# Optimization experiments

Measured on AMD Instinct MI355X. Metric: run time of the kernel, lower is better.

## Reference

```python
import jax, jax.numpy as jnp
import numpy as np

B, T, C = 16, 2048, 1024
HEAD = 64

def setup_inputs() -> dict:
    key = jax.random.key(0)
    kx, kq, kk, kv = jax.random.split(key, 4)
    x = jax.random.normal(kx, (B, T, C), dtype=jnp.float32)
    s = 1.0 / np.sqrt(C)
    Wq = jax.random.normal(kq, (C, HEAD), dtype=jnp.float32) * s
    Wk = jax.random.normal(kk, (C, HEAD), dtype=jnp.float32) * s
    Wv = jax.random.normal(kv, (C, HEAD), dtype=jnp.float32) * s
    return {"x": x, "Wq": Wq, "Wk": Wk, "Wv": Wv}

def reference(x, Wq, Wk, Wv):
    Bb, Tt, Cc = x.shape
    q = jnp.einsum('btc,ch->bth', x, Wq)  # [B,T,H]
    k = jnp.einsum('btc,ch->bth', x, Wk)
    v = jnp.einsum('btc,ch->bth', x, Wv)
    # NOTE: source scales by C**-0.5 (n_embd), not head_size**-0.5
    scores = jnp.einsum('bth,bsh->bts', q, k) * (Cc ** -0.5)  # [B,T,T]
    causal = jnp.tril(jnp.ones((Tt, Tt), dtype=bool))
    scores = jnp.where(causal, scores, -jnp.inf)
    attn = jax.nn.softmax(scores, axis=-1)  # dropout p=0 -> identity
    out = jnp.einsum('bts,bsh->bth', attn, v)  # [B,T,H]
    return out
```

## Files before the change

kernel.cpp:

```cpp
#include <hip/hip_runtime.h>

typedef __bf16 bf16;
typedef __bf16 bf16x2 __attribute__((ext_vector_type(2)));
typedef __bf16 bf16x4 __attribute__((ext_vector_type(4)));
typedef __bf16 bf16x8 __attribute__((ext_vector_type(8)));
typedef float f32x4 __attribute__((ext_vector_type(4)));

#define TT_ 2048
#define CC_ 1024
#define HH_ 64

#define SCALE2 0.045084221f

static __device__ __forceinline__ unsigned pack_bf16(float a, float b) {
    union { bf16x2 h; unsigned u; } z;
    z.h = bf16x2{(bf16)a, (bf16)b};
    return z.u;
}
static __device__ __forceinline__ void plswap32(unsigned &a, unsigned &b) {
    asm("v_permlane32_swap_b32 %0, %1" : "+v"(a), "+v"(b));
}
static __device__ __forceinline__ void plswap16(unsigned &a, unsigned &b) {
    asm("v_permlane16_swap_b32 %0, %1" : "+v"(a), "+v"(b));
}

__global__ __launch_bounds__(256) void prep_w(const float* __restrict__ Wq,
                                              const float* __restrict__ Wk,
                                              const float* __restrict__ Wv,
                                              bf16* __restrict__ Wt) {
    __shared__ bf16 Ls[64 * 65];
    const int m  = blockIdx.x >> 4;
    const int k0 = (blockIdx.x & 15) * 64;
    const float* W = (m == 0) ? Wq : (m == 1) ? Wk : Wv;
    const int tid = threadIdx.x;
    #pragma unroll
    for (int j = 0; j < 4; ++j) {
        int idx = tid + 256 * j;
        int r   = idx >> 4;
        int c4  = (idx & 15) * 4;
        float4 w = *(const float4*)&W[(size_t)(k0 + r) * HH_ + c4];
        Ls[r * 65 + c4 + 0] = (bf16)w.x;
        Ls[r * 65 + c4 + 1] = (bf16)w.y;
        Ls[r * 65 + c4 + 2] = (bf16)w.z;
        Ls[r * 65 + c4 + 3] = (bf16)w.w;
    }
    __syncthreads();
    #pragma unroll
    for (int j = 0; j < 4; ++j) {
        int idx = tid + 256 * j;
        int n   = idx >> 4;
        int kc  = (idx & 15) * 4;
        bf16x4 v;
        #pragma unroll
        for (int i = 0; i < 4; ++i) v[i] = Ls[(kc + i) * 65 + n];
        *(bf16x4*)&Wt[m * 65536 + n * 1024 + k0 + kc] = v;
    }
}

#define QKV_STEP(KBI, BU, BP, XLD, XWR)                                        \
    {                                                                          \
        const int k0 = (KBI) * 64;                                             \
        __syncthreads();                                                       \
        if ((KBI) < 14) {                                                      \
            _Pragma("unroll")                                                  \
            for (int rr = 0; rr < 4; ++rr)                                     \
                XLD[rr] = *(const float4*)&x[(size_t)(m0 + srow + rr * 16) * CC_ + k0 + 128 + scol]; \
        }                                                                      \
        if ((KBI) < 15) {                                                      \
            _Pragma("unroll")                                                  \
            for (int step = 0; step < 2; ++step)                               \
                _Pragma("unroll")                                              \
                for (int ct = 0; ct < 3; ++ct)                                 \
                    BP[step][ct] = *(const bf16x8*)&Wt[(size_t)(wave * 48 + ct * 16 + lane) * 1024 + k0 + 64 + step * 32 + quad * 8]; \
        }                                                                      \
        bf16x8 afr[2][4];                                                      \
        _Pragma("unroll")                                                      \
        for (int step = 0; step < 2; ++step)                                   \
            _Pragma("unroll")                                                  \
            for (int rt = 0; rt < 4; ++rt)                                     \
                afr[step][rt] = *(const bf16x8*)&Xs[(KBI) & 1][(rt * 16 + lane) * 72 + step * 32 + quad * 8]; \
        _Pragma("unroll")                                                      \
        for (int step = 0; step < 2; ++step)                                   \
            _Pragma("unroll")                                                  \
            for (int ct = 0; ct < 3; ++ct)                                     \
                _Pragma("unroll")                                              \
                for (int rt = 0; rt < 4; ++rt)                                 \
                    acc[rt][ct] = __builtin_amdgcn_mfma_f32_16x16x32_bf16(afr[step][rt], BU[step][ct], acc[rt][ct], 0, 0, 0); \
        if ((KBI) < 15) {                                                      \
            _Pragma("unroll")                                                  \
            for (int rr = 0; rr < 4; ++rr) {                                   \
                bf16x4 bv = {(bf16)XWR[rr].x, (bf16)XWR[rr].y, (bf16)XWR[rr].z, (bf16)XWR[rr].w}; \
                *(bf16x4*)&Xs[((KBI) + 1) & 1][(srow + rr * 16) * 72 + scol] = bv; \
            }                                                                  \
        }                                                                      \
    }

__global__ __launch_bounds__(256, 2) void qkv_kernel(const float* __restrict__ x,
                                                     const bf16* __restrict__ Wt,
                                                     bf16* __restrict__ qb,
                                                     bf16* __restrict__ kb,
                                                     bf16* __restrict__ vt) {
    __shared__ __align__(16) bf16 Xs[2][64 * 72];
    const int tid  = threadIdx.x;
    const int wave = tid >> 6;
    const int lane = tid & 15;
    const int quad = (tid & 63) >> 4;
    const int m0   = blockIdx.x * 64;

    f32x4 acc[4][3];
    #pragma unroll
    for (int i = 0; i < 4; ++i)
        #pragma unroll
        for (int j = 0; j < 3; ++j) acc[i][j] = f32x4{0.f, 0.f, 0.f, 0.f};

    const int srow = tid >> 4;
    const int scol = (tid & 15) * 4;

    {
        float4 x0[4];
        #pragma unroll
        for (int rr = 0; rr < 4; ++rr)
            x0[rr] = *(const float4*)&x[(size_t)(m0 + srow + rr * 16) * CC_ + scol];
        #pragma unroll
        for (int rr = 0; rr < 4; ++rr) {
            bf16x4 bv = {(bf16)x0[rr].x, (bf16)x0[rr].y, (bf16)x0[rr].z, (bf16)x0[rr].w};
            *(bf16x4*)&Xs[0][(srow + rr * 16) * 72 + scol] = bv;
        }
    }
    float4 xS0[4], xS1[4];
    #pragma unroll
    for (int rr = 0; rr < 4; ++rr)
        xS1[rr] = *(const float4*)&x[(size_t)(m0 + srow + rr * 16) * CC_ + 64 + scol];
    bf16x8 bfrA[2][3], bfrB[2][3];
    #pragma unroll
    for (int step = 0; step < 2; ++step)
        #pragma unroll
        for (int ct = 0; ct < 3; ++ct)
            bfrA[step][ct] = *(const bf16x8*)&Wt[(size_t)(wave * 48 + ct * 16 + lane) * 1024 + step * 32 + quad * 8];

    for (int kb2 = 0; kb2 < 16; kb2 += 2) {
        QKV_STEP(kb2,     bfrA, bfrB, xS0, xS1)
        QKV_STEP(kb2 + 1, bfrB, bfrA, xS1, xS0)
    }

    const int bb = m0 >> 11;
    const int t0 = m0 & 2047;
    __syncthreads();
    #pragma unroll
    for (int ct = 0; ct < 3; ++ct) {
        int c0 = wave * 48 + ct * 16;
        if (c0 < 64) {
            int h = c0 + lane;
            #pragma unroll
            for (int rt = 0; rt < 4; ++rt)
                #pragma unroll
                for (int r = 0; r < 4; ++r)
                    qb[(size_t)(m0 + rt * 16 + quad * 4 + r) * HH_ + h] = (bf16)(acc[rt][ct][r] * SCALE2);
        } else if (c0 < 128) {
            int h = (c0 - 64) + lane;
            #pragma unroll
            for (int rt = 0; rt < 4; ++rt)
                #pragma unroll
                for (int r = 0; r < 4; ++r)
                    kb[(size_t)(m0 + rt * 16 + quad * 4 + r) * HH_ + h] = (bf16)acc[rt][ct][r];
        } else {
            int h = (c0 - 128) + lane;
            #pragma unroll
            for (int rt = 0; rt < 4; ++rt)
                #pragma unroll
                for (int r = 0; r < 4; ++r)
                    Xs[0][(rt * 16 + quad * 4 + r) * 72 + h] = (bf16)acc[rt][ct][r];
        }
    }
    __syncthreads();
    {
        int h  = tid >> 2;
        int tc = (tid & 3) * 16;
        bf16x8 v0, v1;
        #pragma unroll
        for (int i = 0; i < 8; ++i) v0[i] = Xs[0][(tc + i) * 72 + h];
        #pragma unroll
        for (int i = 0; i < 8; ++i) v1[i] = Xs[0][(tc + 8 + i) * 72 + h];
        bf16* dst = &vt[(size_t)bb * HH_ * TT_ + (size_t)h * TT_ + t0 + tc];
        *(bf16x8*)dst = v0;
        *(bf16x8*)(dst + 8) = v1;
    }
}

__global__ __launch_bounds__(256, 2) void attn_kernel(const bf16* __restrict__ qb,
                                                      const bf16* __restrict__ kb,
                                                      const bf16* __restrict__ vt,
                                                      float* __restrict__ out) {
    __shared__ __align__(16) bf16 Ks[2][128 * 72];
    __shared__ __align__(16) bf16 Vs[2][64 * 136];

    const int tid  = threadIdx.x;
    const int wave = tid >> 6;
    const int lane = tid & 15;
    const int quad = (tid & 63) >> 4;

    const int j  = blockIdx.x;
    const int bb = j & 15;
    const int p  = j >> 4;
    const int qi = (p < 16) ? p : 47 - p;
    const int nch = (qi >> 1) + 1;

    const int qrow  = qi * 64 + wave * 16;
    const int qg    = qrow + lane;
    const int qmaxw = qrow + 15;

    const int krow = tid >> 3, kc8 = (tid & 7) * 8;
    const int vh   = tid >> 4, vc8 = (tid & 15) * 8;
    const bf16* kp = kb + (size_t)(bb * TT_ + krow) * HH_ + kc8;
    const bf16* vp = vt + (size_t)bb * HH_ * TT_ + (size_t)vh * TT_ + vc8;

    bf16x8 kr[4], vvr[4];
    #pragma unroll
    for (int j2 = 0; j2 < 4; ++j2) kr[j2]  = *(const bf16x8*)&kp[(size_t)j2 * 32 * HH_];
    #pragma unroll
    for (int j2 = 0; j2 < 4; ++j2) vvr[j2] = *(const bf16x8*)&vp[j2 * 16 * TT_];
    #pragma unroll
    for (int j2 = 0; j2 < 4; ++j2) *(bf16x8*)&Ks[0][(krow + 32 * j2) * 72 + kc8] = kr[j2];
    #pragma unroll
    for (int j2 = 0; j2 < 4; ++j2) *(bf16x8*)&Vs[0][(vh + 16 * j2) * 136 + vc8]  = vvr[j2];
    __syncthreads();

    bf16x8 aq[2];
    #pragma unroll
    for (int step = 0; step < 2; ++step)
        aq[step] = *(const bf16x8*)&qb[(size_t)(bb * TT_ + qg) * HH_ + step * 32 + quad * 8];

    bf16x8 vones;
    #pragma unroll
    for (int i = 0; i < 8; ++i) vones[i] = (bf16)1.0f;

    f32x4 o_acc[4];
    #pragma unroll
    for (int ht = 0; ht < 4; ++ht) o_acc[ht] = f32x4{0.f, 0.f, 0.f, 0.f};
    f32x4 lacc = f32x4{0.f, 0.f, 0.f, 0.f};

    for (int c = 0; c < nch; ++c) {
        const int s0  = c * 128;
        const int cur = c & 1;
        if (c + 1 < nch) {
            #pragma unroll
            for (int j2 = 0; j2 < 4; ++j2)
                kr[j2] = *(const bf16x8*)&kp[(size_t)((c + 1) * 128 + j2 * 32) * HH_];
            #pragma unroll
            for (int j2 = 0; j2 < 4; ++j2)
                vvr[j2] = *(const bf16x8*)&vp[(c + 1) * 128 + j2 * 16 * TT_];
        }

        const bool msk = (c == nch - 1);
        #pragma unroll
        for (int w = 0; w < 4; ++w) {
            if (msk && (s0 + w * 32 > qmaxw)) continue;
            const bool haveB = !msk || (s0 + w * 32 + 16 <= qmaxw);

            f32x4 sA = {0.f, 0.f, 0.f, 0.f};
            f32x4 sB = {0.f, 0.f, 0.f, 0.f};
            __builtin_amdgcn_s_setprio(1);
            {
                bf16x8 ak0 = *(const bf16x8*)&Ks[cur][(w * 32 + lane) * 72 + quad * 8];
                bf16x8 ak1 = *(const bf16x8*)&Ks[cur][(w * 32 + lane) * 72 + 32 + quad * 8];
                sA = __builtin_amdgcn_mfma_f32_16x16x32_bf16(ak0, aq[0], sA, 0, 0, 0);
                sA = __builtin_amdgcn_mfma_f32_16x16x32_bf16(ak1, aq[1], sA, 0, 0, 0);
            }
            if (haveB) {
                bf16x8 bk0 = *(const bf16x8*)&Ks[cur][(w * 32 + 16 + lane) * 72 + quad * 8];
                bf16x8 bk1 = *(const bf16x8*)&Ks[cur][(w * 32 + 16 + lane) * 72 + 32 + quad * 8];
                sB = __builtin_amdgcn_mfma_f32_16x16x32_bf16(bk0, aq[0], sB, 0, 0, 0);
                sB = __builtin_amdgcn_mfma_f32_16x16x32_bf16(bk1, aq[1], sB, 0, 0, 0);
            }
            __builtin_amdgcn_s_setprio(0);

            const int kA0 = s0 + w * 32 + quad * 4;
            float eA[4], eB[4];
            #pragma unroll
            for (int r = 0; r < 4; ++r) {
                float e = __builtin_amdgcn_exp2f(sA[r]);
                if (msk && (kA0 + r > qg)) e = 0.f;
                eA[r] = e;
            }
            if (haveB) {
                #pragma unroll
                for (int r = 0; r < 4; ++r) {
                    float e = __builtin_amdgcn_exp2f(sB[r]);
                    if (msk && (kA0 + 16 + r > qg)) e = 0.f;
                    eB[r] = e;
                }
            } else {
                #pragma unroll
                for (int r = 0; r < 4; ++r) eB[r] = 0.f;
            }

            unsigned d0 = pack_bf16(eA[0], eA[1]);
            unsigned d1 = pack_bf16(eA[2], eA[3]);
            unsigned d2 = pack_bf16(eB[0], eB[1]);
            unsigned d3 = pack_bf16(eB[2], eB[3]);
            plswap32(d0, d2);
            plswap16(d0, d2);
            plswap32(d1, d3);
            plswap16(d1, d3);
            union { unsigned u[4]; bf16x8 v; } apu;
            apu.u[0] = d0; apu.u[1] = d1; apu.u[2] = d2; apu.u[3] = d3;

            __builtin_amdgcn_s_setprio(1);
            #pragma unroll
            for (int ht = 0; ht < 4; ++ht) {
                bf16x8 bv = *(const bf16x8*)&Vs[cur][(ht * 16 + lane) * 136 + w * 32 + quad * 8];
                o_acc[ht] = __builtin_amdgcn_mfma_f32_16x16x32_bf16(apu.v, bv, o_acc[ht], 0, 0, 0);
            }
            lacc = __builtin_amdgcn_mfma_f32_16x16x32_bf16(apu.v, vones, lacc, 0, 0, 0);
            __builtin_amdgcn_s_setprio(0);
        }

        if (c + 1 < nch) {
            #pragma unroll
            for (int j2 = 0; j2 < 4; ++j2) *(bf16x8*)&Ks[cur ^ 1][(krow + 32 * j2) * 72 + kc8] = kr[j2];
            #pragma unroll
            for (int j2 = 0; j2 < 4; ++j2) *(bf16x8*)&Vs[cur ^ 1][(vh + 16 * j2) * 136 + vc8]  = vvr[j2];
            __syncthreads();
        }
    }

    float inv[4];
    #pragma unroll
    for (int r = 0; r < 4; ++r) inv[r] = __builtin_amdgcn_rcpf(lacc[r]);
    #pragma unroll
    for (int ht = 0; ht < 4; ++ht)
        #pragma unroll
        for (int r = 0; r < 4; ++r)
            out[(size_t)(bb * TT_ + qrow + quad * 4 + r) * HH_ + ht * 16 + lane] = o_acc[ht][r] * inv[r];
}

extern "C" void kernel_launch(void* const* d_in, const int* in_sizes, int n_in,
                              void* d_out, int out_size, void* d_ws, size_t ws_size,
                              hipStream_t stream) {
    const float* x  = (const float*)d_in[0];
    const float* Wq = (const float*)d_in[1];
    const float* Wk = (const float*)d_in[2];
    const float* Wv = (const float*)d_in[3];
    float* out = (float*)d_out;

    char* ws = (char*)d_ws;
    bf16*  qb = (bf16*)(ws);
    bf16*  kb = (bf16*)(ws + 4194304);
    bf16*  vt = (bf16*)(ws + 8388608);
    bf16*  Wt = (bf16*)(ws + 12582912);

    prep_w<<<48, 256, 0, stream>>>(Wq, Wk, Wv, Wt);
    qkv_kernel<<<512, 256, 0, stream>>>(x, Wt, qb, kb, vt);
    attn_kernel<<<512, 256, 0, stream>>>(qb, kb, vt, out);
}
```

Baseline: 238.5 us.

## Split key chunks across two wave groups in attention and reduce via LDS

Doubles the attention block to 512 threads: four query waves are paired with two key groups, and each group handles alternating 32-key sub-tiles of every 128-key chunk. Partial output and row-sum accumulators are then combined through shared memory before normalisation. The aim is more waves per block to hide latency and to halve the serial per-wave work on the long causal rows. The cost is an extra LDS reduction with two barriers, and the launch-bounds change to (512,4) constrains register allocation more tightly.

```diff
diff --git a/kernel.cpp b/kernel.cpp
--- a/kernel.cpp
+++ b/kernel.cpp
@@ -187,7 +187,7 @@
     }
 }
 
-__global__ __launch_bounds__(256, 2) void attn_kernel(const bf16* __restrict__ qb,
+__global__ __launch_bounds__(512, 4) void attn_kernel(const bf16* __restrict__ qb,
                                                       const bf16* __restrict__ kb,
                                                       const bf16* __restrict__ vt,
                                                       float* __restrict__ out) {
@@ -196,6 +196,8 @@
 
     const int tid  = threadIdx.x;
     const int wave = tid >> 6;
+    const int qw   = wave & 3;
+    const int kg   = wave >> 2;
     const int lane = tid & 15;
     const int quad = (tid & 63) >> 4;
 
@@ -205,7 +207,7 @@
     const int qi = (p < 16) ? p : 47 - p;
     const int nch = (qi >> 1) + 1;
 
-    const int qrow  = qi * 64 + wave * 16;
+    const int qrow  = qi * 64 + qw * 16;
     const int qg    = qrow + lane;
     const int qmaxw = qrow + 15;
 
@@ -214,15 +216,15 @@
     const bf16* kp = kb + (size_t)(bb * TT_ + krow) * HH_ + kc8;
     const bf16* vp = vt + (size_t)bb * HH_ * TT_ + (size_t)vh * TT_ + vc8;
 
-    bf16x8 kr[4], vvr[4];
-    #pragma unroll
-    for (int j2 = 0; j2 < 4; ++j2) kr[j2]  = *(const bf16x8*)&kp[(size_t)j2 * 32 * HH_];
-    #pragma unroll
-    for (int j2 = 0; j2 < 4; ++j2) vvr[j2] = *(const bf16x8*)&vp[j2 * 16 * TT_];
-    #pragma unroll
-    for (int j2 = 0; j2 < 4; ++j2) *(bf16x8*)&Ks[0][(krow + 32 * j2) * 72 + kc8] = kr[j2];
-    #pragma unroll
-    for (int j2 = 0; j2 < 4; ++j2) *(bf16x8*)&Vs[0][(vh + 16 * j2) * 136 + vc8]  = vvr[j2];
+    bf16x8 kr[2], vvr[2];
+    #pragma unroll
+    for (int j2 = 0; j2 < 2; ++j2) kr[j2]  = *(const bf16x8*)&kp[(size_t)j2 * 64 * HH_];
+    #pragma unroll
+    for (int j2 = 0; j2 < 2; ++j2) vvr[j2] = *(const bf16x8*)&vp[j2 * 32 * TT_];
+    #pragma unroll
+    for (int j2 = 0; j2 < 2; ++j2) *(bf16x8*)&Ks[0][(krow + 64 * j2) * 72 + kc8] = kr[j2];
+    #pragma unroll
+    for (int j2 = 0; j2 < 2; ++j2) *(bf16x8*)&Vs[0][(vh + 32 * j2) * 136 + vc8]  = vvr[j2];
     __syncthreads();
 
     bf16x8 aq[2];
@@ -244,16 +246,17 @@
         const int cur = c & 1;
         if (c + 1 < nch) {
             #pragma unroll
-            for (int j2 = 0; j2 < 4; ++j2)
-                kr[j2] = *(const bf16x8*)&kp[(size_t)((c + 1) * 128 + j2 * 32) * HH_];
-            #pragma unroll
-            for (int j2 = 0; j2 < 4; ++j2)
-                vvr[j2] = *(const bf16x8*)&vp[(c + 1) * 128 + j2 * 16 * TT_];
+            for (int j2 = 0; j2 < 2; ++j2)
+                kr[j2] = *(const bf16x8*)&kp[(size_t)((c + 1) * 128 + j2 * 64) * HH_];
+            #pragma unroll
+            for (int j2 = 0; j2 < 2; ++j2)
+                vvr[j2] = *(const bf16x8*)&vp[(c + 1) * 128 + j2 * 32 * TT_];
         }
 
         const bool msk = (c == nch - 1);
         #pragma unroll
-        for (int w = 0; w < 4; ++w) {
+        for (int wi = 0; wi < 2; ++wi) {
+            const int w = kg + wi * 2;
             if (msk && (s0 + w * 32 > qmaxw)) continue;
             const bool haveB = !msk || (s0 + w * 32 + 16 <= qmaxw);
 
@@ -317,21 +320,44 @@
 
         if (c + 1 < nch) {
             #pragma unroll
-            for (int j2 = 0; j2 < 4; ++j2) *(bf16x8*)&Ks[cur ^ 1][(krow + 32 * j2) * 72 + kc8] = kr[j2];
-            #pragma unroll
-            for (int j2 = 0; j2 < 4; ++j2) *(bf16x8*)&Vs[cur ^ 1][(vh + 16 * j2) * 136 + vc8]  = vvr[j2];
+            for (int j2 = 0; j2 < 2; ++j2) *(bf16x8*)&Ks[cur ^ 1][(krow + 64 * j2) * 72 + kc8] = kr[j2];
+            #pragma unroll
+            for (int j2 = 0; j2 < 2; ++j2) *(bf16x8*)&Vs[cur ^ 1][(vh + 32 * j2) * 136 + vc8]  = vvr[j2];
             __syncthreads();
         }
     }
 
-    float inv[4];
-    #pragma unroll
-    for (int r = 0; r < 4; ++r) inv[r] = __builtin_amdgcn_rcpf(lacc[r]);
-    #pragma unroll
-    for (int ht = 0; ht < 4; ++ht)
+    __syncthreads();
+    float* cbuf = (float*)&Ks[0][0];
+    float* lbuf = cbuf + 64 * 65;
+    if (kg == 1) {
+        #pragma unroll
+        for (int ht = 0; ht < 4; ++ht)
+            #pragma unroll
+            for (int r = 0; r < 4; ++r)
+                cbuf[(qw * 16 + quad * 4 + r) * 65 + ht * 16 + lane] = o_acc[ht][r];
+        if (lane == 0) {
+            #pragma unroll
+            for (int r = 0; r < 4; ++r) lbuf[qw * 16 + quad * 4 + r] = lacc[r];
+        }
+    }
+    __syncthreads();
+    if (kg == 0) {
+        #pragma unroll
+        for (int ht = 0; ht < 4; ++ht)
+            #pragma unroll
+            for (int r = 0; r < 4; ++r)
+                o_acc[ht][r] += cbuf[(qw * 16 + quad * 4 + r) * 65 + ht * 16 + lane];
+        float inv[4];
         #pragma unroll
         for (int r = 0; r < 4; ++r)
-            out[(size_t)(bb * TT_ + qrow + quad * 4 + r) * HH_ + ht * 16 + lane] = o_acc[ht][r] * inv[r];
+            inv[r] = __builtin_amdgcn_rcpf(lacc[r] + lbuf[qw * 16 + quad * 4 + r]);
+        #pragma unroll
+        for (int ht = 0; ht < 4; ++ht)
+            #pragma unroll
+            for (int r = 0; r < 4; ++r)
+                out[(size_t)(bb * TT_ + qrow + quad * 4 + r) * HH_ + ht * 16 + lane] = o_acc[ht][r] * inv[r];
+    }
 }
 
 extern "C" void kernel_launch(void* const* d_in, const int* in_sizes, int n_in,
@@ -351,5 +377,5 @@
 
     prep_w<<<48, 256, 0, stream>>>(Wq, Wk, Wv, Wt);
     qkv_kernel<<<512, 256, 0, stream>>>(x, Wt, qb, kb, vt);
-    attn_kernel<<<512, 256, 0, stream>>>(qb, kb, vt, out);
-}
+    attn_kernel<<<512, 512, 0, stream>>>(qb, kb, vt, out);
+}
```

Measured after the change: 232.1 us. 1.03x faster.
